# Kernel tuning notes

Hardware: AMD Instinct MI355X
Metric: run time of the kernel (lower is better)

## Reference

```python
import jax, jax.numpy as jnp
import numpy as np

B, Q, K, D = 32, 1024, 1024, 64
MASK_VAL = -1000000.0  # matches torch source's -1e6 fill


def setup_inputs() -> dict:
    key = jax.random.key(0)
    kq, kk, kv, kl = jax.random.split(key, 4)
    return {
        "queries": jax.random.normal(kq, (B, Q, D), dtype=jnp.float32),
        "keys": jax.random.normal(kk, (B, K, D), dtype=jnp.float32),
        "values": jax.random.normal(kv, (B, K, D), dtype=jnp.float32),
        "valid_lens": jax.random.randint(kl, (B,), 1, K + 1, dtype=jnp.int64),
    }


def reference(queries, keys, values, valid_lens):
    d = queries.shape[-1]
    # [B, Q, K] scores
    scores = jnp.einsum("bqd,bkd->bqk", queries, keys) / jnp.sqrt(jnp.asarray(d, queries.dtype))
    # 1D valid_lens -> same length mask for every query row of a batch element
    kv_pos = jnp.arange(scores.shape[-1])  # [K]
    mask = kv_pos[None, None, :] < valid_lens[:, None, None]  # [B, 1, K] broadcast
    scores = jnp.where(mask, scores, MASK_VAL)
    attn = jax.nn.softmax(scores, axis=-1)
    # dropout p=0.0 -> identity
    return jnp.einsum("bqk,bkd->bqd", attn, values)
```

## Files before the change

### kernel.cpp

```cpp
#include <hip/hip_runtime.h>
#include <hip/hip_bf16.h>

#define NB 32
#define NQ 1024
#define NK 1024
#define ND 64
#define M_FIX 16.0f

typedef __attribute__((ext_vector_type(8))) __bf16 bf16x8;
typedef __attribute__((ext_vector_type(8))) short  s16x8;
typedef __attribute__((ext_vector_type(4))) short  s16x4;
typedef __attribute__((ext_vector_type(4))) float  f32x4;
typedef __attribute__((ext_vector_type(4))) int    i32x4;
typedef __attribute__((ext_vector_type(2))) int    i32x2;

static __device__ __forceinline__ short f2bf(float f) {
  unsigned u = __builtin_bit_cast(unsigned, f);
  u += 0x7fffu + ((u >> 16) & 1u);
  return (short)(u >> 16);
}

#define GLD_LDS16(gp, lp)                                              \
  __builtin_amdgcn_global_load_lds(                                    \
      (const __attribute__((address_space(1))) void*)(gp),             \
      (__attribute__((address_space(3))) void*)(lp), 16, 0, 0)

#define MFMA16(acc, va_, vb_)                                          \
  asm("v_mfma_f32_16x16x16_bf16 %0, %1, %2, %0"                        \
      : "+v"(acc) : "v"(va_), "v"(vb_))

__launch_bounds__(256)
__global__ void prep_kv(const float* __restrict__ Kp, const float* __restrict__ Vp,
                        const int* __restrict__ VLp,
                        short* __restrict__ Kb, short* __restrict__ Vt) {
  __shared__ __align__(16) short T[64 * 72];
  const int wg = blockIdx.x;
  const int b  = wg >> 4;
  const int kt = wg & 15;

  const bool is64 = (VLp[1] == 0);
  const int  len  = is64 ? VLp[2 * b] : VLp[b];
  if (kt * 64 >= len) return;

  const int tid = threadIdx.x;

  {
    const int key = tid >> 2, d0 = (tid & 3) * 16, g0 = (tid & 3) * 2;
    const int row = key & 31, st = key >> 5;
    const float* src = Kp + ((size_t)(b * NK + kt * 64 + key)) * ND + d0;
    short out[16];
#pragma unroll
    for (int i = 0; i < 16; i += 4) {
      float4 v = *(const float4*)(src + i);
      out[i] = f2bf(v.x); out[i + 1] = f2bf(v.y);
      out[i + 2] = f2bf(v.z); out[i + 3] = f2bf(v.w);
    }
    short* dtile = Kb + ((size_t)(b * 32 + kt * 2 + st)) * 2048;
    *(s16x8*)&dtile[row * 64 + (((g0    ) ^ (row & 7)) << 3)] = *(const s16x8*)out;
    *(s16x8*)&dtile[row * 64 + (((g0 + 1) ^ (row & 7)) << 3)] = *(const s16x8*)(out + 8);
  }

  {
    const int vkey = tid & 63, vd0 = (tid >> 6) * 16;
    const float* src = Vp + ((size_t)(b * NK + kt * 64 + vkey)) * ND + vd0;
#pragma unroll
    for (int i = 0; i < 4; ++i) {
      float4 v = *(const float4*)(src + i * 4);
      T[(vd0 + i * 4 + 0) * 72 + vkey] = f2bf(v.x);
      T[(vd0 + i * 4 + 1) * 72 + vkey] = f2bf(v.y);
      T[(vd0 + i * 4 + 2) * 72 + vkey] = f2bf(v.z);
      T[(vd0 + i * 4 + 3) * 72 + vkey] = f2bf(v.w);
    }
  }
  __syncthreads();
  {
    const int d = tid >> 2, q4 = tid & 3;
    const int st = q4 >> 1, half = q4 & 1;
    short* vtile = Vt + ((size_t)(b * 32 + kt * 2 + st)) * 2048;
    const short* s = &T[d * 72 + q4 * 16];
#pragma unroll
    for (int g = 0; g < 4; ++g)
      *(s16x4*)&vtile[d * 32 + (((g ^ (d & 3)) & 3) << 3) + half * 4] =
          *(const s16x4*)(s + 4 * g);
  }
}

__launch_bounds__(512, 4)
__global__ void attn_fwd(const float* __restrict__ Qp,
                         const short* __restrict__ Kb,
                         const short* __restrict__ Vt,
                         const int* __restrict__ VLp,
                         float* __restrict__ Op) {
  __shared__ __align__(16) short SM[24576];
  char* smb = (char*)SM;

  const int wg  = blockIdx.x;
  const int swz = (wg & 7) * 64 + (wg >> 3);
  const int b   = swz >> 4;
  const int qb  = swz & 15;

  const int tid  = threadIdx.x;
  const int wid  = tid >> 6;
  const int lane = tid & 63;
  const int l16  = lane & 15;
  const int grp  = lane >> 4;
  const int esw  = l16 & 7;
  const int e3   = l16 & 3;
  const int qgrp = wid >> 1;
  const int par  = wid & 1;

  const bool is64 = (VLp[1] == 0);
  const int  len  = is64 ? VLp[2 * b] : VLp[b];
  const int  ntiles = (len + 31) >> 5;
  const int  nsup   = (ntiles + 1) >> 1;
  const int  remLast = len - ((ntiles - 1) << 5);

  const float qscale = 0.125f * 1.44269504088896341f;

  bf16x8 qf[2];
  {
    const float* qsrc = Qp + ((size_t)(b * NQ + qb * 64 + qgrp * 16 + l16)) * ND + grp * 8;
#pragma unroll
    for (int k2 = 0; k2 < 2; ++k2) {
      float4 a = *(const float4*)(qsrc + k2 * 32);
      float4 c = *(const float4*)(qsrc + k2 * 32 + 4);
      s16x8 t;
      t[0] = f2bf(a.x * qscale); t[1] = f2bf(a.y * qscale);
      t[2] = f2bf(a.z * qscale); t[3] = f2bf(a.w * qscale);
      t[4] = f2bf(c.x * qscale); t[5] = f2bf(c.y * qscale);
      t[6] = f2bf(c.z * qscale); t[7] = f2bf(c.w * qscale);
      qf[k2] = __builtin_bit_cast(bf16x8, t);
    }
  }

  const int kOff0 = par * 4096 + l16 * 128 + (((0 + grp) ^ esw) << 4);
  const int kOff1 = par * 4096 + l16 * 128 + (((4 + grp) ^ esw) << 4);
  const int vOff  = par * 4096 + l16 * 64 + ((((grp ^ e3) & 3)) << 4);

  const char* kgp = (const char*)(Kb + (size_t)b * 32 * 2048) + tid * 16;
  const char* vgp = (const char*)(Vt + (size_t)b * 32 * 2048) + tid * 16;
  const int dstW = wid * 1024;

  const f32x4 minit = {-M_FIX, -M_FIX, -M_FIX, -M_FIX};
  const f32x4 vzero = {0.f, 0.f, 0.f, 0.f};
  f32x4 oacc[4];
#pragma unroll
  for (int i = 0; i < 4; ++i) oacc[i] = vzero;
  float lrun = 0.f;

  GLD_LDS16(kgp, smb + dstW);
  GLD_LDS16(vgp, smb + 24576 + dstW);
  kgp += 8192; vgp += 8192;
  if (nsup > 1) {
    GLD_LDS16(kgp, smb + 8192 + dstW);
    GLD_LDS16(vgp, smb + 32768 + dstW);
    kgp += 8192; vgp += 8192;
  }

  int kbCur = 0;
  int kbDst = 16384;

  for (int it = 0; it < nsup; ++it) {
    if (it + 1 < nsup) {
      asm volatile("s_waitcnt vmcnt(2)" ::: "memory");
    } else {
      asm volatile("s_waitcnt vmcnt(0)" ::: "memory");
    }
    __builtin_amdgcn_sched_barrier(0);
    __builtin_amdgcn_s_barrier();
    __builtin_amdgcn_sched_barrier(0);

    if (it + 2 < nsup) {
      GLD_LDS16(kgp, smb + kbDst + dstW);
      GLD_LDS16(vgp, smb + 24576 + kbDst + dstW);
      kgp += 8192; vgp += 8192;
    }

    const int myt = 2 * it + par;
    if (myt < ntiles) {
      f32x4 sc[2];
      __builtin_amdgcn_s_setprio(1);
#pragma unroll
      for (int n = 0; n < 2; ++n) {
        bf16x8 kf0 = __builtin_bit_cast(bf16x8,
            *(const s16x8*)(smb + kbCur + kOff0 + n * 2048));
        bf16x8 kf1 = __builtin_bit_cast(bf16x8,
            *(const s16x8*)(smb + kbCur + kOff1 + n * 2048));
        f32x4 acc = __builtin_amdgcn_mfma_f32_16x16x32_bf16(kf0, qf[0], minit, 0, 0, 0);
        acc = __builtin_amdgcn_mfma_f32_16x16x32_bf16(kf1, qf[1], acc, 0, 0, 0);
        sc[n] = acc;
      }
      __builtin_amdgcn_s_setprio(0);

      i32x2 pk[2];
      if (myt == ntiles - 1) {
#pragma unroll
        for (int n = 0; n < 2; ++n) {
#pragma unroll
          for (int r = 0; r < 4; ++r) {
            float x = (n * 16 + grp * 4 + r < remLast) ? sc[n][r] : -128.0f;
            float pv = exp2f(x);
            sc[n][r] = pv;
            lrun += pv;
          }
          int plo, phi;
          asm("v_cvt_pk_bf16_f32 %0, %1, %2" : "=v"(plo) : "v"(sc[n][0]), "v"(sc[n][1]));
          asm("v_cvt_pk_bf16_f32 %0, %1, %2" : "=v"(phi) : "v"(sc[n][2]), "v"(sc[n][3]));
          pk[n][0] = plo; pk[n][1] = phi;
        }
      } else {
#pragma unroll
        for (int n = 0; n < 2; ++n) {
#pragma unroll
          for (int r = 0; r < 4; ++r) {
            float pv = exp2f(sc[n][r]);
            sc[n][r] = pv;
            lrun += pv;
          }
          int plo, phi;
          asm("v_cvt_pk_bf16_f32 %0, %1, %2" : "=v"(plo) : "v"(sc[n][0]), "v"(sc[n][1]));
          asm("v_cvt_pk_bf16_f32 %0, %1, %2" : "=v"(phi) : "v"(sc[n][2]), "v"(sc[n][3]));
          pk[n][0] = plo; pk[n][1] = phi;
        }
      }
      __builtin_amdgcn_sched_barrier(0);

      __builtin_amdgcn_s_setprio(1);
#pragma unroll
      for (int m = 0; m < 4; ++m) {
        i32x4 w = *(const i32x4*)(smb + 24576 + kbCur + vOff + m * 1024);
        i32x2 vlo = {w[0], w[1]};
        i32x2 vhi = {w[2], w[3]};
        MFMA16(oacc[m], vlo, pk[0]);
        MFMA16(oacc[m], vhi, pk[1]);
      }
      __builtin_amdgcn_s_setprio(0);
    }

    kbCur = (kbCur == 16384) ? 0 : kbCur + 8192;
    kbDst = (kbDst == 16384) ? 0 : kbDst + 8192;
  }

  __builtin_amdgcn_sched_barrier(0);
  asm volatile("s_nop 7\n\ts_nop 7" ::: "memory");

  __syncthreads();
  float* CB = (float*)SM;
  const int crow = qgrp * 64 + lane;
  if (par == 1) {
    float* dst = CB + (size_t)crow * 20;
#pragma unroll
    for (int m = 0; m < 4; ++m) *(f32x4*)(dst + m * 4) = oacc[m];
    dst[16] = lrun;
  }
  __syncthreads();
  if (par == 0) {
    const float* src = CB + (size_t)crow * 20;
#pragma unroll
    for (int m = 0; m < 4; ++m) oacc[m] += *(const f32x4*)(src + m * 4);
    float l = lrun + src[16];
    l += __shfl_xor(l, 16);
    l += __shfl_xor(l, 32);
    const float inv = 1.0f / l;

    float* obase = Op + ((size_t)(b * NQ + qb * 64 + qgrp * 16 + l16)) * ND;
#pragma unroll
    for (int m = 0; m < 4; ++m) {
      float4 o = {oacc[m][0] * inv, oacc[m][1] * inv,
                  oacc[m][2] * inv, oacc[m][3] * inv};
      *(float4*)(obase + m * 16 + grp * 4) = o;
    }
  }
}

extern "C" void kernel_launch(void* const* d_in, const int* in_sizes, int n_in,
                              void* d_out, int out_size, void* d_ws, size_t ws_size,
                              hipStream_t stream) {
  const float* Qp = (const float*)d_in[0];
  const float* Kp = (const float*)d_in[1];
  const float* Vp = (const float*)d_in[2];
  const int*   VL = (const int*)d_in[3];
  float* Op = (float*)d_out;

  short* Kb = (short*)d_ws;
  short* Vt = Kb + (size_t)NB * NK * ND;

  prep_kv<<<dim3(NB * 16), dim3(256), 0, stream>>>(Kp, Vp, VL, Kb, Vt);
  attn_fwd<<<dim3(NB * 16), dim3(512), 0, stream>>>(Qp, Kb, Vt, VL, Op);
}
```

Before: 30.04 us.

## Halve attention workgroup size and switch to double-buffered K/V staging

Each workgroup now handles 32 query rows with 256 threads instead of 64 rows with 512 threads, doubling the grid to improve CU fill and occupancy. The triple-buffered LDS ring for K/V tiles is replaced by a double buffer with a full vmcnt(0) wait each iteration, shrinking LDS use. This trades more blocks per CU against doubled K/V global/LDS traffic per query and less load/compute overlap.

Result: no change. 30.03 us (-0.0%).

```diff
diff --git a/kernel.cpp b/kernel.cpp
--- a/kernel.cpp
+++ b/kernel.cpp
@@ -85,19 +85,19 @@
   }
 }
 
-__launch_bounds__(512, 4)
+__launch_bounds__(256, 5)
 __global__ void attn_fwd(const float* __restrict__ Qp,
                          const short* __restrict__ Kb,
                          const short* __restrict__ Vt,
                          const int* __restrict__ VLp,
                          float* __restrict__ Op) {
-  __shared__ __align__(16) short SM[24576];
+  __shared__ __align__(16) short SM[16384];
   char* smb = (char*)SM;
 
   const int wg  = blockIdx.x;
-  const int swz = (wg & 7) * 64 + (wg >> 3);
-  const int b   = swz >> 4;
-  const int qb  = swz & 15;
+  const int swz = (wg & 7) * 128 + (wg >> 3);
+  const int b   = swz >> 5;
+  const int qb  = swz & 31;
 
   const int tid  = threadIdx.x;
   const int wid  = tid >> 6;
@@ -119,7 +119,7 @@
 
   bf16x8 qf[2];
   {
-    const float* qsrc = Qp + ((size_t)(b * NQ + qb * 64 + qgrp * 16 + l16)) * ND + grp * 8;
+    const float* qsrc = Qp + ((size_t)(b * NQ + qb * 32 + qgrp * 16 + l16)) * ND + grp * 8;
 #pragma unroll
     for (int k2 = 0; k2 < 2; ++k2) {
       float4 a = *(const float4*)(qsrc + k2 * 32);
@@ -135,44 +135,38 @@
 
   const int kOff0 = par * 4096 + l16 * 128 + (((0 + grp) ^ esw) << 4);
   const int kOff1 = par * 4096 + l16 * 128 + (((4 + grp) ^ esw) << 4);
-  const int vOff  = par * 4096 + l16 * 64 + ((((grp ^ e3) & 3)) << 4);
+  const int vOff  = 8192 + par * 4096 + l16 * 64 + (((grp ^ e3) & 3) << 4);
 
   const char* kgp = (const char*)(Kb + (size_t)b * 32 * 2048) + tid * 16;
   const char* vgp = (const char*)(Vt + (size_t)b * 32 * 2048) + tid * 16;
   const int dstW = wid * 1024;
 
   const f32x4 minit = {-M_FIX, -M_FIX, -M_FIX, -M_FIX};
-  const f32x4 vzero = {0.f, 0.f, 0.f, 0.f};
   f32x4 oacc[4];
 #pragma unroll
-  for (int i = 0; i < 4; ++i) oacc[i] = vzero;
+  for (int i = 0; i < 4; ++i) oacc[i] = {0.f, 0.f, 0.f, 0.f};
   float lrun = 0.f;
 
-  GLD_LDS16(kgp, smb + dstW);
-  GLD_LDS16(vgp, smb + 24576 + dstW);
+  int bufB = 0;
+
+  GLD_LDS16(kgp,        smb + dstW);
+  GLD_LDS16(kgp + 4096, smb + 4096 + dstW);
+  GLD_LDS16(vgp,        smb + 8192 + dstW);
+  GLD_LDS16(vgp + 4096, smb + 12288 + dstW);
   kgp += 8192; vgp += 8192;
-  if (nsup > 1) {
-    GLD_LDS16(kgp, smb + 8192 + dstW);
-    GLD_LDS16(vgp, smb + 32768 + dstW);
-    kgp += 8192; vgp += 8192;
-  }
-
-  int kbCur = 0;
-  int kbDst = 16384;
 
   for (int it = 0; it < nsup; ++it) {
-    if (it + 1 < nsup) {
-      asm volatile("s_waitcnt vmcnt(2)" ::: "memory");
-    } else {
-      asm volatile("s_waitcnt vmcnt(0)" ::: "memory");
-    }
+    asm volatile("s_waitcnt vmcnt(0)" ::: "memory");
     __builtin_amdgcn_sched_barrier(0);
     __builtin_amdgcn_s_barrier();
     __builtin_amdgcn_sched_barrier(0);
 
-    if (it + 2 < nsup) {
-      GLD_LDS16(kgp, smb + kbDst + dstW);
-      GLD_LDS16(vgp, smb + 24576 + kbDst + dstW);
+    if (it + 1 < nsup) {
+      const int nb = bufB ^ 16384;
+      GLD_LDS16(kgp,        smb + nb + dstW);
+      GLD_LDS16(kgp + 4096, smb + nb + 4096 + dstW);
+      GLD_LDS16(vgp,        smb + nb + 8192 + dstW);
+      GLD_LDS16(vgp + 4096, smb + nb + 12288 + dstW);
       kgp += 8192; vgp += 8192;
     }
 
@@ -183,9 +177,9 @@
 #pragma unroll
       for (int n = 0; n < 2; ++n) {
         bf16x8 kf0 = __builtin_bit_cast(bf16x8,
-            *(const s16x8*)(smb + kbCur + kOff0 + n * 2048));
+            *(const s16x8*)(smb + bufB + kOff0 + n * 2048));
         bf16x8 kf1 = __builtin_bit_cast(bf16x8,
-            *(const s16x8*)(smb + kbCur + kOff1 + n * 2048));
+            *(const s16x8*)(smb + bufB + kOff1 + n * 2048));
         f32x4 acc = __builtin_amdgcn_mfma_f32_16x16x32_bf16(kf0, qf[0], minit, 0, 0, 0);
         acc = __builtin_amdgcn_mfma_f32_16x16x32_bf16(kf1, qf[1], acc, 0, 0, 0);
         sc[n] = acc;
@@ -228,7 +222,7 @@
       __builtin_amdgcn_s_setprio(1);
 #pragma unroll
       for (int m = 0; m < 4; ++m) {
-        i32x4 w = *(const i32x4*)(smb + 24576 + kbCur + vOff + m * 1024);
+        i32x4 w = *(const i32x4*)(smb + bufB + vOff + m * 1024);
         i32x2 vlo = {w[0], w[1]};
         i32x2 vhi = {w[2], w[3]};
         MFMA16(oacc[m], vlo, pk[0]);
@@ -237,8 +231,7 @@
       __builtin_amdgcn_s_setprio(0);
     }
 
-    kbCur = (kbCur == 16384) ? 0 : kbCur + 8192;
-    kbDst = (kbDst == 16384) ? 0 : kbDst + 8192;
+    bufB ^= 16384;
   }
 
   __builtin_amdgcn_sched_barrier(0);
@@ -263,7 +256,7 @@
     l += __shfl_xor(l, 32);
     const float inv = 1.0f / l;
 
-    float* obase = Op + ((size_t)(b * NQ + qb * 64 + qgrp * 16 + l16)) * ND;
+    float* obase = Op + ((size_t)(b * NQ + qb * 32 + qgrp * 16 + l16)) * ND;
 #pragma unroll
     for (int m = 0; m < 4; ++m) {
       float4 o = {oacc[m][0] * inv, oacc[m][1] * inv,
@@ -286,5 +279,5 @@
   short* Vt = Kb + (size_t)NB * NK * ND;
 
   prep_kv<<<dim3(NB * 16), dim3(256), 0, stream>>>(Kp, Vp, VL, Kb, Vt);
-  attn_fwd<<<dim3(NB * 16), dim3(512), 0, stream>>>(Qp, Kb, Vt, VL, Op);
-}
+  attn_fwd<<<dim3(NB * 32), dim3(256), 0, stream>>>(Qp, Kb, Vt, VL, Op);
+}
```
